# Kernel optimization log

Measured on AMD Instinct MI355X. Metric: run time of the kernel, lower is better.

The kernel has to match this reference:

```python
import jax, jax.numpy as jnp
import numpy as np

WIN = 8          # window_size
DIM = 96         # embedding dim
HEADS = 3        # num_heads
N = WIN * WIN    # tokens per window
B_ = 8192        # total windows (2 images * 64*64 windows)
NUM_WIN = 4096   # windows per image (mask leading dim)


def _relative_position_index():
    # Same construction as the torch module (meshgrid default 'ij').
    ch = np.arange(WIN)
    coords = np.stack(np.meshgrid(ch, ch, indexing="ij"))          # [2, W, W]
    flat = coords.reshape(2, -1)                                     # [2, N]
    rel = flat[:, :, None] - flat[:, None, :]                        # [2, N, N]
    rel = rel.transpose(1, 2, 0).astype(np.int32)                    # [N, N, 2]
    rel[:, :, 0] += WIN - 1
    rel[:, :, 1] += WIN - 1
    rel[:, :, 0] *= 2 * WIN - 1
    return rel.sum(-1)                                               # [N, N] int32


def setup_inputs() -> dict:
    key = jax.random.key(0)
    ks = jax.random.split(key, 8)
    x = jax.random.normal(ks[0], (B_, N, DIM), dtype=jnp.float32)
    mask = jax.random.normal(ks[1], (NUM_WIN, N, N), dtype=jnp.float32)
    s = 0.02
    qkv_w = jax.random.normal(ks[2], (3 * DIM, DIM), dtype=jnp.float32) * s
    qkv_b = jax.random.normal(ks[3], (3 * DIM,), dtype=jnp.float32) * s
    proj_w = jax.random.normal(ks[4], (DIM, DIM), dtype=jnp.float32) * s
    proj_b = jax.random.normal(ks[5], (DIM,), dtype=jnp.float32) * s
    n_bias = (2 * WIN - 1) * (2 * WIN - 1)  # 225
    bias_table = jax.random.normal(ks[6], (n_bias, HEADS), dtype=jnp.float32) * s
    rel_idx = jnp.asarray(_relative_position_index())  # [N, N] int32
    return {"x": x, "mask": mask, "qkv_w": qkv_w, "qkv_b": qkv_b,
            "proj_w": proj_w, "proj_b": proj_b, "bias_table": bias_table,
            "rel_idx": rel_idx}


def reference(x, mask, qkv_w, qkv_b, proj_w, proj_b, bias_table, rel_idx):
    Bw, n, C = x.shape
    hd = C // HEADS
    scale = hd ** (-0.5)
    qkv = (x @ qkv_w.T + qkv_b).reshape(Bw, n, 3, HEADS, hd)
    qkv = jnp.transpose(qkv, (2, 0, 3, 1, 4))
    q, k, v = qkv[0], qkv[1], qkv[2]
    attn = jnp.einsum("bhqd,bhkd->bhqk", q * scale, k)              # [Bw, H, n, n]
    # relative position bias gather: [n, n, H] -> [H, n, n]
    bias = bias_table[rel_idx.reshape(-1)].reshape(n, n, HEADS)
    attn = attn + jnp.transpose(bias, (2, 0, 1))[None]
    # shift mask: broadcast over (batch, heads)
    nw = mask.shape[0]
    attn = attn.reshape(Bw // nw, nw, HEADS, n, n) + mask[None, :, None]
    attn = attn.reshape(Bw, HEADS, n, n)
    attn = jax.nn.softmax(attn, axis=-1)
    out = jnp.einsum("bhqk,bhkd->bhqd", attn, v)                    # [Bw, H, n, hd]
    out = jnp.transpose(out, (0, 2, 1, 3)).reshape(Bw, n, C)
    return out @ proj_w.T + proj_b
```

## Files before the change

### kernel.cpp

```cpp
#include <hip/hip_runtime.h>

typedef __attribute__((ext_vector_type(8))) short short8v;
typedef __attribute__((ext_vector_type(4))) float f32x4;

__device__ __forceinline__ ushort f2bf(float f) {
  union { float f; unsigned int u; } c; c.f = f;
  return (ushort)((c.u + 0x7FFFu + ((c.u >> 16) & 1u)) >> 16);
}

__device__ __forceinline__ unsigned cvtpk(float a, float b) {
  unsigned r;
  asm("v_cvt_pk_bf16_f32 %0, %1, %2" : "=v"(r) : "v"(a), "v"(b));
  return r;
}

__device__ __forceinline__ short8v bits8(unsigned a, unsigned b, unsigned c, unsigned d) {
  union { unsigned u[4]; short8v s; } cv;
  cv.u[0] = a; cv.u[1] = b; cv.u[2] = c; cv.u[3] = d;
  return cv.s;
}

__global__ __launch_bounds__(256) void setup_k(
    const float* __restrict__ qkv_w, const float* __restrict__ proj_w,
    const float* __restrict__ bias_table, const int* __restrict__ rel_idx,
    const float* __restrict__ qkv_b,
    ushort* __restrict__ qkv_wb, ushort* __restrict__ proj_wb,
    float* __restrict__ bias_comb, float* __restrict__ qkv_bs) {
  const float qs = 0.17677669529663687f;
  int idx = blockIdx.x * 256 + threadIdx.x;
  if (idx < 27648) {
    qkv_wb[idx] = f2bf(qkv_w[idx] * (idx < 9216 ? qs : 1.0f));
  } else if (idx < 36864) {
    int i = idx - 27648;
    proj_wb[i] = f2bf(proj_w[i]);
  } else if (idx < 49152) {
    int i = idx - 36864;
    int h = i / 4096, rc = i % 4096;
    bias_comb[i] = bias_table[rel_idx[rc] * 3 + h];
  } else if (idx < 49440) {
    int i = idx - 49152;
    qkv_bs[i] = qkv_b[i] * (i < 96 ? qs : 1.0f);
  }
}

__global__ __launch_bounds__(256, 3) void winattn(
    const float* __restrict__ x, const float* __restrict__ mask,
    const ushort* __restrict__ qkv_wb, const ushort* __restrict__ proj_wb,
    const float* __restrict__ bias_comb, const float* __restrict__ qkv_bs,
    const float* __restrict__ proj_b, float* __restrict__ out) {
  __shared__ ushort klds[2][64][104];
  __shared__ ushort vts[2][96][72];

  const int bb = blockIdx.x;
  const int t = threadIdx.x;
  const int w = t >> 6;
  const int lane = t & 63;
  const int l15 = lane & 15;
  const int g = lane >> 4;
  const int qrow = w * 16 + l15;

  short8v xa[2][3];
  #pragma unroll
  for (int u = 0; u < 2; ++u) {
    const float* xr = x + ((size_t)(bb + u * 4096) * 64 + qrow) * 96 + g * 8;
    #pragma unroll
    for (int ks3 = 0; ks3 < 3; ++ks3) {
      float4 a0 = *reinterpret_cast<const float4*>(xr + ks3 * 32);
      float4 a1 = *reinterpret_cast<const float4*>(xr + ks3 * 32 + 4);
      xa[u][ks3] = bits8(cvtpk(a0.x, a0.y), cvtpk(a0.z, a0.w),
                         cvtpk(a1.x, a1.y), cvtpk(a1.z, a1.w));
    }
  }

  #pragma unroll
  for (int nt = 0; nt < 6; ++nt) {
    short8v bf[3];
    #pragma unroll
    for (int ks3 = 0; ks3 < 3; ++ks3)
      bf[ks3] = *reinterpret_cast<const short8v*>(qkv_wb + (nt * 16 + l15) * 96 + ks3 * 32 + g * 8);
    float4 qb = *reinterpret_cast<const float4*>(qkv_bs + nt * 16 + g * 4);
    #pragma unroll
    for (int u = 0; u < 2; ++u) {
      f32x4 acc = {0.f, 0.f, 0.f, 0.f};
      #pragma unroll
      for (int ks3 = 0; ks3 < 3; ++ks3)
        acc = __builtin_amdgcn_mfma_f32_16x16x32_bf16(bf[ks3], xa[u][ks3], acc, 0, 0, 0);
      uint2 pk = make_uint2(cvtpk(acc[0] + qb.x, acc[1] + qb.y),
                            cvtpk(acc[2] + qb.z, acc[3] + qb.w));
      *reinterpret_cast<uint2*>(&klds[u][qrow][nt * 16 + g * 4]) = pk;
    }
  }
  asm volatile("" ::: "memory");
  short8v qf[2][3];
  #pragma unroll
  for (int u = 0; u < 2; ++u)
    #pragma unroll
    for (int h = 0; h < 3; ++h)
      qf[u][h] = *reinterpret_cast<const short8v*>(&klds[u][qrow][h * 32 + g * 8]);
  asm volatile("" ::: "memory");

  #pragma unroll
  for (int nt = 6; nt < 12; ++nt) {
    short8v bf[3];
    #pragma unroll
    for (int ks3 = 0; ks3 < 3; ++ks3)
      bf[ks3] = *reinterpret_cast<const short8v*>(qkv_wb + (nt * 16 + l15) * 96 + ks3 * 32 + g * 8);
    float4 qb = *reinterpret_cast<const float4*>(qkv_bs + nt * 16 + g * 4);
    #pragma unroll
    for (int u = 0; u < 2; ++u) {
      f32x4 acc = {0.f, 0.f, 0.f, 0.f};
      #pragma unroll
      for (int ks3 = 0; ks3 < 3; ++ks3)
        acc = __builtin_amdgcn_mfma_f32_16x16x32_bf16(bf[ks3], xa[u][ks3], acc, 0, 0, 0);
      uint2 pk = make_uint2(cvtpk(acc[0] + qb.x, acc[1] + qb.y),
                            cvtpk(acc[2] + qb.z, acc[3] + qb.w));
      *reinterpret_cast<uint2*>(&klds[u][qrow][(nt - 6) * 16 + g * 4]) = pk;
    }
  }

  #pragma unroll
  for (int nt = 12; nt < 18; ++nt) {
    const int cw = nt * 16 + l15;
    short8v bf[3];
    #pragma unroll
    for (int ks3 = 0; ks3 < 3; ++ks3)
      bf[ks3] = *reinterpret_cast<const short8v*>(qkv_wb + cw * 96 + ks3 * 32 + g * 8);
    const float vb = qkv_bs[cw];
    #pragma unroll
    for (int u = 0; u < 2; ++u) {
      f32x4 acc = {0.f, 0.f, 0.f, 0.f};
      #pragma unroll
      for (int ks3 = 0; ks3 < 3; ++ks3)
        acc = __builtin_amdgcn_mfma_f32_16x16x32_bf16(xa[u][ks3], bf[ks3], acc, 0, 0, 0);
      uint2 pk = make_uint2(cvtpk(acc[0] + vb, acc[1] + vb),
                            cvtpk(acc[2] + vb, acc[3] + vb));
      *reinterpret_cast<uint2*>(&vts[u][cw - 192][w * 16 + g * 4]) = pk;
    }
  }
  __syncthreads();

  const bool ghi = (g >= 2);
  const int srcA = l15 + 16 * ((g & 1) * 2);
  const int srcB = srcA + 16;

  f32x4 pacc[2][6];
  #pragma unroll
  for (int u = 0; u < 2; ++u)
    #pragma unroll
    for (int nt2 = 0; nt2 < 6; ++nt2) pacc[u][nt2] = (f32x4){0.f, 0.f, 0.f, 0.f};

  const float* mrow = mask + (size_t)bb * 4096 + qrow * 64;
  const float* bcb0 = bias_comb + qrow * 64;

  #pragma unroll
  for (int h = 0; h < 3; ++h) {
    short8v pfw[6];
    #pragma unroll
    for (int nt2 = 0; nt2 < 6; ++nt2)
      pfw[nt2] = *reinterpret_cast<const short8v*>(proj_wb + (nt2 * 16 + l15) * 96 + h * 32 + g * 8);

    f32x4 s[2][4];
    #pragma unroll
    for (int tj = 0; tj < 4; ++tj) {
      #pragma unroll
      for (int u = 0; u < 2; ++u) {
        short8v kf = *reinterpret_cast<const short8v*>(&klds[u][tj * 16 + l15][h * 32 + g * 8]);
        f32x4 z = {0.f, 0.f, 0.f, 0.f};
        s[u][tj] = __builtin_amdgcn_mfma_f32_16x16x32_bf16(kf, qf[u][h], z, 0, 0, 0);
      }
    }
    #pragma unroll
    for (int tj = 0; tj < 4; ++tj) {
      float4 bc4 = *reinterpret_cast<const float4*>(bcb0 + h * 4096 + tj * 16 + g * 4);
      float4 mk4 = *reinterpret_cast<const float4*>(mrow + tj * 16 + g * 4);
      float bm[4] = {bc4.x + mk4.x, bc4.y + mk4.y, bc4.z + mk4.z, bc4.w + mk4.w};
      #pragma unroll
      for (int u = 0; u < 2; ++u)
        #pragma unroll
        for (int r = 0; r < 4; ++r) s[u][tj][r] += bm[r];
    }
    float inv[2];
    #pragma unroll
    for (int u = 0; u < 2; ++u) {
      #pragma unroll
      for (int tj = 0; tj < 4; ++tj)
        #pragma unroll
        for (int r = 0; r < 4; ++r) s[u][tj][r] = __expf(s[u][tj][r]);
      float sm = ((s[u][0][0] + s[u][0][1]) + (s[u][0][2] + s[u][0][3]))
               + ((s[u][1][0] + s[u][1][1]) + (s[u][1][2] + s[u][1][3]))
               + ((s[u][2][0] + s[u][2][1]) + (s[u][2][2] + s[u][2][3]))
               + ((s[u][3][0] + s[u][3][1]) + (s[u][3][2] + s[u][3][3]));
      sm += __shfl_xor(sm, 16);
      sm += __shfl_xor(sm, 32);
      inv[u] = __builtin_amdgcn_rcpf(sm);
    }
    unsigned ppk[2][4][2];
    #pragma unroll
    for (int u = 0; u < 2; ++u)
      #pragma unroll
      for (int tj = 0; tj < 4; ++tj) {
        ppk[u][tj][0] = cvtpk(s[u][tj][0], s[u][tj][1]);
        ppk[u][tj][1] = cvtpk(s[u][tj][2], s[u][tj][3]);
      }
    short8v pfv[2][2];
    #pragma unroll
    for (int u = 0; u < 2; ++u)
      #pragma unroll
      for (int ks2 = 0; ks2 < 2; ++ks2) {
        unsigned dm[4];
        #pragma unroll
        for (int m = 0; m < 4; ++m) {
          const int sl = (m < 2) ? srcA : srcB;
          unsigned lo = __shfl(ppk[u][ks2 * 2 + 0][m & 1], sl);
          unsigned hi = __shfl(ppk[u][ks2 * 2 + 1][m & 1], sl);
          dm[m] = ghi ? hi : lo;
        }
        pfv[u][ks2] = bits8(dm[0], dm[1], dm[2], dm[3]);
      }
    f32x4 oacc[2][2];
    #pragma unroll
    for (int u = 0; u < 2; ++u)
      #pragma unroll
      for (int nt = 0; nt < 2; ++nt) {
        f32x4 o = {0.f, 0.f, 0.f, 0.f};
        #pragma unroll
        for (int ks2 = 0; ks2 < 2; ++ks2) {
          short8v vf = *reinterpret_cast<const short8v*>(&vts[u][h * 32 + nt * 16 + l15][ks2 * 32 + g * 8]);
          o = __builtin_amdgcn_mfma_f32_16x16x32_bf16(vf, pfv[u][ks2], o, 0, 0, 0);
        }
        oacc[u][nt] = o;
      }
    short8v ofv[2];
    #pragma unroll
    for (int u = 0; u < 2; ++u) {
      unsigned opk[2][2];
      #pragma unroll
      for (int nt = 0; nt < 2; ++nt) {
        opk[nt][0] = cvtpk(oacc[u][nt][0] * inv[u], oacc[u][nt][1] * inv[u]);
        opk[nt][1] = cvtpk(oacc[u][nt][2] * inv[u], oacc[u][nt][3] * inv[u]);
      }
      unsigned dm[4];
      #pragma unroll
      for (int m = 0; m < 4; ++m) {
        const int sl = (m < 2) ? srcA : srcB;
        unsigned lo = __shfl(opk[0][m & 1], sl);
        unsigned hi = __shfl(opk[1][m & 1], sl);
        dm[m] = ghi ? hi : lo;
      }
      ofv[u] = bits8(dm[0], dm[1], dm[2], dm[3]);
    }
    #pragma unroll
    for (int nt2 = 0; nt2 < 6; ++nt2)
      #pragma unroll
      for (int u = 0; u < 2; ++u)
        pacc[u][nt2] = __builtin_amdgcn_mfma_f32_16x16x32_bf16(ofv[u], pfw[nt2], pacc[u][nt2], 0, 0, 0);
  }

  float pb[6];
  #pragma unroll
  for (int nt2 = 0; nt2 < 6; ++nt2) pb[nt2] = proj_b[nt2 * 16 + l15];
  #pragma unroll
  for (int u = 0; u < 2; ++u) {
    float* ob = out + (size_t)(bb + u * 4096) * 6144 + (w * 16 + g * 4) * 96 + l15;
    #pragma unroll
    for (int nt2 = 0; nt2 < 6; ++nt2)
      #pragma unroll
      for (int r = 0; r < 4; ++r)
        ob[r * 96 + nt2 * 16] = pacc[u][nt2][r] + pb[nt2];
  }
}

extern "C" void kernel_launch(void* const* d_in, const int* in_sizes, int n_in,
                              void* d_out, int out_size, void* d_ws, size_t ws_size,
                              hipStream_t stream) {
  const float* x          = (const float*)d_in[0];
  const float* mask       = (const float*)d_in[1];
  const float* qkv_w      = (const float*)d_in[2];
  const float* qkv_b      = (const float*)d_in[3];
  const float* proj_w     = (const float*)d_in[4];
  const float* proj_b     = (const float*)d_in[5];
  const float* bias_table = (const float*)d_in[6];
  const int*   rel_idx    = (const int*)d_in[7];

  char* ws = (char*)d_ws;
  ushort* qkv_wb    = (ushort*)ws;
  ushort* proj_wb   = (ushort*)(ws + 55296);
  float*  bias_comb = (float*)(ws + 55296 + 18432);
  float*  qkv_bs    = (float*)(ws + 55296 + 18432 + 49152);

  setup_k<<<194, 256, 0, stream>>>(qkv_w, proj_w, bias_table, rel_idx, qkv_b,
                                   qkv_wb, proj_wb, bias_comb, qkv_bs);
  winattn<<<4096, 256, 0, stream>>>(x, mask, qkv_wb, proj_wb,
                                    bias_comb, qkv_bs, proj_b, (float*)d_out);
}
```

Before: 176.8 us.

## Use exp2 softmax, register-shuffle Q, swizzle V LDS, and defer output projection

Folds log2(e) into the Q scale, bias table and mask so the softmax can use a native exp2 instead of __expf. Q fragments are now built with lane shuffles from registers rather than a round trip through LDS. V^T in LDS loses its padding and uses an XOR swizzle to avoid bank conflicts. The mask is prefetched before the barrier, and the output projection is moved after all three heads so the proj weights are loaded in a separate phase. This trades more live registers (ofv across heads, mask values) for fewer LDS and global-load stalls inside the head loop, which may cost occupancy.

After: 180.2 us. About the same (+1.9%).

```diff
diff --git a/kernel.cpp b/kernel.cpp
--- a/kernel.cpp
+++ b/kernel.cpp
@@ -2,6 +2,8 @@
 
 typedef __attribute__((ext_vector_type(8))) short short8v;
 typedef __attribute__((ext_vector_type(4))) float f32x4;
+
+#define INVLN2 1.4426950408889634f
 
 __device__ __forceinline__ ushort f2bf(float f) {
   union { float f; unsigned int u; } c; c.f = f;
@@ -12,6 +14,14 @@
   unsigned r;
   asm("v_cvt_pk_bf16_f32 %0, %1, %2" : "=v"(r) : "v"(a), "v"(b));
   return r;
+}
+
+__device__ __forceinline__ float exp2w(float x) {
+#if __has_builtin(__builtin_amdgcn_exp2f)
+  return __builtin_amdgcn_exp2f(x);
+#else
+  return __expf(x * 0.6931471805599453f);
+#endif
 }
 
 __device__ __forceinline__ short8v bits8(unsigned a, unsigned b, unsigned c, unsigned d) {
@@ -26,7 +36,7 @@
     const float* __restrict__ qkv_b,
     ushort* __restrict__ qkv_wb, ushort* __restrict__ proj_wb,
     float* __restrict__ bias_comb, float* __restrict__ qkv_bs) {
-  const float qs = 0.17677669529663687f;
+  const float qs = 0.17677669529663687f * INVLN2;
   int idx = blockIdx.x * 256 + threadIdx.x;
   if (idx < 27648) {
     qkv_wb[idx] = f2bf(qkv_w[idx] * (idx < 9216 ? qs : 1.0f));
@@ -36,7 +46,7 @@
   } else if (idx < 49152) {
     int i = idx - 36864;
     int h = i / 4096, rc = i % 4096;
-    bias_comb[i] = bias_table[rel_idx[rc] * 3 + h];
+    bias_comb[i] = bias_table[rel_idx[rc] * 3 + h] * INVLN2;
   } else if (idx < 49440) {
     int i = idx - 49152;
     qkv_bs[i] = qkv_b[i] * (i < 96 ? qs : 1.0f);
@@ -49,7 +59,7 @@
     const float* __restrict__ bias_comb, const float* __restrict__ qkv_bs,
     const float* __restrict__ proj_b, float* __restrict__ out) {
   __shared__ ushort klds[2][64][104];
-  __shared__ ushort vts[2][96][72];
+  __shared__ ushort vts[2][96][64];
 
   const int bb = blockIdx.x;
   const int t = threadIdx.x;
@@ -59,6 +69,10 @@
   const int g = lane >> 4;
   const int qrow = w * 16 + l15;
 
+  const bool ghi = (g >= 2);
+  const int srcA = l15 + 16 * ((g & 1) * 2);
+  const int srcB = srcA + 16;
+
   short8v xa[2][3];
   #pragma unroll
   for (int u = 0; u < 2; ++u) {
@@ -72,6 +86,7 @@
     }
   }
 
+  unsigned qpk[2][6][2];
   #pragma unroll
   for (int nt = 0; nt < 6; ++nt) {
     short8v bf[3];
@@ -85,19 +100,25 @@
       #pragma unroll
       for (int ks3 = 0; ks3 < 3; ++ks3)
         acc = __builtin_amdgcn_mfma_f32_16x16x32_bf16(bf[ks3], xa[u][ks3], acc, 0, 0, 0);
-      uint2 pk = make_uint2(cvtpk(acc[0] + qb.x, acc[1] + qb.y),
-                            cvtpk(acc[2] + qb.z, acc[3] + qb.w));
-      *reinterpret_cast<uint2*>(&klds[u][qrow][nt * 16 + g * 4]) = pk;
-    }
-  }
-  asm volatile("" ::: "memory");
+      qpk[u][nt][0] = cvtpk(acc[0] + qb.x, acc[1] + qb.y);
+      qpk[u][nt][1] = cvtpk(acc[2] + qb.z, acc[3] + qb.w);
+    }
+  }
   short8v qf[2][3];
   #pragma unroll
   for (int u = 0; u < 2; ++u)
     #pragma unroll
-    for (int h = 0; h < 3; ++h)
-      qf[u][h] = *reinterpret_cast<const short8v*>(&klds[u][qrow][h * 32 + g * 8]);
-  asm volatile("" ::: "memory");
+    for (int h = 0; h < 3; ++h) {
+      unsigned dm[4];
+      #pragma unroll
+      for (int m = 0; m < 4; ++m) {
+        const int sl = (m < 2) ? srcA : srcB;
+        unsigned lo = __shfl(qpk[u][2 * h + 0][m & 1], sl);
+        unsigned hi = __shfl(qpk[u][2 * h + 1][m & 1], sl);
+        dm[m] = ghi ? hi : lo;
+      }
+      qf[u][h] = bits8(dm[0], dm[1], dm[2], dm[3]);
+    }
 
   #pragma unroll
   for (int nt = 6; nt < 12; ++nt) {
@@ -121,6 +142,8 @@
   #pragma unroll
   for (int nt = 12; nt < 18; ++nt) {
     const int cw = nt * 16 + l15;
+    const int vc = cw - 192;
+    const int tk = (w * 16 + g * 4) ^ ((vc & 7) << 3);
     short8v bf[3];
     #pragma unroll
     for (int ks3 = 0; ks3 < 3; ++ks3)
@@ -134,31 +157,26 @@
         acc = __builtin_amdgcn_mfma_f32_16x16x32_bf16(xa[u][ks3], bf[ks3], acc, 0, 0, 0);
       uint2 pk = make_uint2(cvtpk(acc[0] + vb, acc[1] + vb),
                             cvtpk(acc[2] + vb, acc[3] + vb));
-      *reinterpret_cast<uint2*>(&vts[u][cw - 192][w * 16 + g * 4]) = pk;
-    }
-  }
+      *reinterpret_cast<uint2*>(&vts[u][vc][tk]) = pk;
+    }
+  }
+
+  const float* mrow = mask + (size_t)bb * 4096 + qrow * 64;
+  float mk[4][4];
+  #pragma unroll
+  for (int tj = 0; tj < 4; ++tj) {
+    float4 m4 = *reinterpret_cast<const float4*>(mrow + tj * 16 + g * 4);
+    mk[tj][0] = m4.x * INVLN2; mk[tj][1] = m4.y * INVLN2;
+    mk[tj][2] = m4.z * INVLN2; mk[tj][3] = m4.w * INVLN2;
+  }
+
   __syncthreads();
 
-  const bool ghi = (g >= 2);
-  const int srcA = l15 + 16 * ((g & 1) * 2);
-  const int srcB = srcA + 16;
-
-  f32x4 pacc[2][6];
-  #pragma unroll
-  for (int u = 0; u < 2; ++u)
-    #pragma unroll
-    for (int nt2 = 0; nt2 < 6; ++nt2) pacc[u][nt2] = (f32x4){0.f, 0.f, 0.f, 0.f};
-
-  const float* mrow = mask + (size_t)bb * 4096 + qrow * 64;
   const float* bcb0 = bias_comb + qrow * 64;
+  short8v ofv[3][2];
 
   #pragma unroll
   for (int h = 0; h < 3; ++h) {
-    short8v pfw[6];
-    #pragma unroll
-    for (int nt2 = 0; nt2 < 6; ++nt2)
-      pfw[nt2] = *reinterpret_cast<const short8v*>(proj_wb + (nt2 * 16 + l15) * 96 + h * 32 + g * 8);
-
     f32x4 s[2][4];
     #pragma unroll
     for (int tj = 0; tj < 4; ++tj) {
@@ -172,8 +190,8 @@
     #pragma unroll
     for (int tj = 0; tj < 4; ++tj) {
       float4 bc4 = *reinterpret_cast<const float4*>(bcb0 + h * 4096 + tj * 16 + g * 4);
-      float4 mk4 = *reinterpret_cast<const float4*>(mrow + tj * 16 + g * 4);
-      float bm[4] = {bc4.x + mk4.x, bc4.y + mk4.y, bc4.z + mk4.z, bc4.w + mk4.w};
+      float bm[4] = {bc4.x + mk[tj][0], bc4.y + mk[tj][1],
+                     bc4.z + mk[tj][2], bc4.w + mk[tj][3]};
       #pragma unroll
       for (int u = 0; u < 2; ++u)
         #pragma unroll
@@ -185,7 +203,7 @@
       #pragma unroll
       for (int tj = 0; tj < 4; ++tj)
         #pragma unroll
-        for (int r = 0; r < 4; ++r) s[u][tj][r] = __expf(s[u][tj][r]);
+        for (int r = 0; r < 4; ++r) s[u][tj][r] = exp2w(s[u][tj][r]);
       float sm = ((s[u][0][0] + s[u][0][1]) + (s[u][0][2] + s[u][0][3]))
                + ((s[u][1][0] + s[u][1][1]) + (s[u][1][2] + s[u][1][3]))
                + ((s[u][2][0] + s[u][2][1]) + (s[u][2][2] + s[u][2][3]))
@@ -222,15 +240,16 @@
     for (int u = 0; u < 2; ++u)
       #pragma unroll
       for (int nt = 0; nt < 2; ++nt) {
+        const int vc = h * 32 + nt * 16 + l15;
         f32x4 o = {0.f, 0.f, 0.f, 0.f};
         #pragma unroll
         for (int ks2 = 0; ks2 < 2; ++ks2) {
-          short8v vf = *reinterpret_cast<const short8v*>(&vts[u][h * 32 + nt * 16 + l15][ks2 * 32 + g * 8]);
+          const int tk = (ks2 * 32 + g * 8) ^ ((vc & 7) << 3);
+          short8v vf = *reinterpret_cast<const short8v*>(&vts[u][vc][tk]);
           o = __builtin_amdgcn_mfma_f32_16x16x32_bf16(vf, pfv[u][ks2], o, 0, 0, 0);
         }
         oacc[u][nt] = o;
       }
-    short8v ofv[2];
     #pragma unroll
     for (int u = 0; u < 2; ++u) {
       unsigned opk[2][2];
@@ -247,13 +266,24 @@
         unsigned hi = __shfl(opk[1][m & 1], sl);
         dm[m] = ghi ? hi : lo;
       }
-      ofv[u] = bits8(dm[0], dm[1], dm[2], dm[3]);
-    }
-    #pragma unroll
-    for (int nt2 = 0; nt2 < 6; ++nt2)
+      ofv[h][u] = bits8(dm[0], dm[1], dm[2], dm[3]);
+    }
+  }
+
+  f32x4 pacc[2][6];
+  #pragma unroll
+  for (int u = 0; u < 2; ++u)
+    #pragma unroll
+    for (int nt2 = 0; nt2 < 6; ++nt2) pacc[u][nt2] = (f32x4){0.f, 0.f, 0.f, 0.f};
+  #pragma unroll
+  for (int h = 0; h < 3; ++h) {
+    #pragma unroll
+    for (int nt2 = 0; nt2 < 6; ++nt2) {
+      short8v pfw = *reinterpret_cast<const short8v*>(proj_wb + (nt2 * 16 + l15) * 96 + h * 32 + g * 8);
       #pragma unroll
       for (int u = 0; u < 2; ++u)
-        pacc[u][nt2] = __builtin_amdgcn_mfma_f32_16x16x32_bf16(ofv[u], pfw[nt2], pacc[u][nt2], 0, 0, 0);
+        pacc[u][nt2] = __builtin_amdgcn_mfma_f32_16x16x32_bf16(ofv[h][u], pfw, pacc[u][nt2], 0, 0, 0);
+    }
   }
 
   float pb[6];
```
